# Performance work log

Hardware: AMD Instinct MI355X
Metric: run time of the kernel (lower is better)

Reference implementation:

```python
import jax, jax.numpy as jnp
import numpy as np

N_NODES = 50000
N_EDGES = 800000
D_NODE = 64
D_EDGE = 32
D_OUT = 64


def setup_inputs() -> dict:
    key = jax.random.key(0)
    ks = jax.random.split(key, 8)
    node_feats = jax.random.normal(ks[0], (N_NODES, D_NODE), dtype=jnp.float32)
    edge_feats = jax.random.normal(ks[1], (N_EDGES, D_EDGE), dtype=jnp.float32)
    src = jax.random.randint(ks[2], (N_EDGES,), 0, N_NODES, dtype=jnp.int32)
    dst = jax.random.randint(ks[3], (N_EDGES,), 0, N_NODES, dtype=jnp.int32)
    # f_e: Linear(D_NODE + D_EDGE + D_NODE -> D_OUT), f_v: Linear(D_OUT + D_NODE -> D_OUT)
    d_in_e = D_NODE + D_EDGE + D_NODE
    d_in_v = D_OUT + D_NODE
    W_e = jax.random.normal(ks[4], (d_in_e, D_OUT), dtype=jnp.float32) / np.sqrt(d_in_e)
    b_e = jnp.zeros((D_OUT,), dtype=jnp.float32)
    W_v = jax.random.normal(ks[5], (d_in_v, D_OUT), dtype=jnp.float32) / np.sqrt(d_in_v)
    b_v = jnp.zeros((D_OUT,), dtype=jnp.float32)
    return {"node_feats": node_feats, "edge_feats": edge_feats, "src": src, "dst": dst,
            "W_e": W_e, "b_e": b_e, "W_v": W_v, "b_v": b_v}


def reference(node_feats, edge_feats, src, dst, W_e, b_e, W_v, b_v):
    n_nodes = node_feats.shape[0]
    # Edge update: gather src/dst node feats, concat with edge feats, MLP + ReLU
    x_e = jnp.concatenate([node_feats[src], edge_feats, node_feats[dst]], axis=1)  # [E, 2*Dn+De]
    m = jax.nn.relu(x_e @ W_e + b_e)  # [E, D_OUT]
    # Mean aggregation by destination node (DGL 'mean': 0 for isolated nodes)
    msum = jax.ops.segment_sum(m, dst, num_segments=n_nodes)  # [N, D_OUT]
    deg = jax.ops.segment_sum(jnp.ones((dst.shape[0],), dtype=m.dtype), dst, num_segments=n_nodes)
    neigh = jnp.where(deg[:, None] > 0, msum / jnp.maximum(deg[:, None], 1.0), 0.0)
    # Node update MLP
    x_v = jnp.concatenate([neigh, node_feats], axis=1)  # [N, D_OUT + Dn]
    return jax.nn.relu(x_v @ W_v + b_v)
```

## Files before the change

kernel.cpp:

```cpp
#include <hip/hip_runtime.h>

#define DN 64
#define DE 32
#define DO 64
#define NB 256
#define TP 128
#define CH 8

typedef __attribute__((ext_vector_type(8))) short bf16x8;
typedef __attribute__((ext_vector_type(4))) float f32x4;

__device__ inline unsigned pack_bf16(float a, float b) {
    unsigned ua = __float_as_uint(a), ub = __float_as_uint(b);
    ua = (ua + 0x7fffu + ((ua >> 16) & 1u)) >> 16;
    ub = (ub + 0x7fffu + ((ub >> 16) & 1u)) >> 16;
    return ua | (ub << 16);
}
__device__ inline unsigned short bf16_1(float a) {
    unsigned u = __float_as_uint(a);
    return (unsigned short)((u + 0x7fffu + ((u >> 16) & 1u)) >> 16);
}
__device__ inline float bf16f(unsigned short v) {
    return __uint_as_float((unsigned)v << 16);
}

union bfu { unsigned u[4]; bf16x8 v; };

__global__ void __launch_bounds__(256) pre_hist_kernel(
    const float* __restrict__ node, const float* __restrict__ W_e,
    const int* __restrict__ dst,
    unsigned short* __restrict__ PsB, unsigned short* __restrict__ PdB,
    int* __restrict__ cnt, int* __restrict__ rank_,
    int n_nodes, int n_edges)
{
    const int t    = threadIdx.x;
    const int lane = t & 63;
    const int w    = __builtin_amdgcn_readfirstlane((int)(t >> 6));
    const int l15  = lane & 15;
    const int k0   = (lane >> 4) << 3;

    bfu bS[4][2], bD[4][2];
#pragma unroll
    for (int Nt = 0; Nt < 4; ++Nt) {
        const int col = (Nt << 4) | l15;
#pragma unroll
        for (int ks = 0; ks < 2; ++ks) {
            float ws[8], wd[8];
#pragma unroll
            for (int e = 0; e < 8; ++e) {
                ws[e] = W_e[(ks * 32 + k0 + e) * DO + col];
                wd[e] = W_e[(96 + ks * 32 + k0 + e) * DO + col];
            }
#pragma unroll
            for (int q = 0; q < 4; ++q) {
                bS[Nt][ks].u[q] = pack_bf16(ws[2 * q], ws[2 * q + 1]);
                bD[Nt][ks].u[q] = pack_bf16(wd[2 * q], wd[2 * q + 1]);
            }
        }
    }

    const int row0 = blockIdx.x * 64 + w * 16;
    if (row0 < n_nodes) {
        bfu aF[2];
#pragma unroll
        for (int ks = 0; ks < 2; ++ks) {
            const int r = min(row0 + l15, n_nodes - 1);
            const float* __restrict__ p = node + (size_t)r * DN + ks * 32 + k0;
            const float4 f0 = *(const float4*)p;
            const float4 f1 = *(const float4*)(p + 4);
            aF[ks].u[0] = pack_bf16(f0.x, f0.y);
            aF[ks].u[1] = pack_bf16(f0.z, f0.w);
            aF[ks].u[2] = pack_bf16(f1.x, f1.y);
            aF[ks].u[3] = pack_bf16(f1.z, f1.w);
        }
        const int rb = row0 + ((lane >> 4) << 2);
#pragma unroll
        for (int Nt = 0; Nt < 4; ++Nt) {
            const f32x4 z = {0.f, 0.f, 0.f, 0.f};
            f32x4 aS = __builtin_amdgcn_mfma_f32_16x16x32_bf16(aF[0].v, bS[Nt][0].v, z, 0, 0, 0);
            aS = __builtin_amdgcn_mfma_f32_16x16x32_bf16(aF[1].v, bS[Nt][1].v, aS, 0, 0, 0);
            f32x4 aD = __builtin_amdgcn_mfma_f32_16x16x32_bf16(aF[0].v, bD[Nt][0].v, z, 0, 0, 0);
            aD = __builtin_amdgcn_mfma_f32_16x16x32_bf16(aF[1].v, bD[Nt][1].v, aD, 0, 0, 0);
            const int col = (Nt << 4) | l15;
#pragma unroll
            for (int r = 0; r < 4; ++r) {
                if (rb + r < n_nodes) {
                    PsB[(size_t)(rb + r) * DO + col] = bf16_1(aS[r]);
                    PdB[(size_t)(rb + r) * DO + col] = bf16_1(aD[r]);
                }
            }
        }
    }

    const int gt = blockIdx.x * blockDim.x + t;
    const int nt = gridDim.x * blockDim.x;
    for (int e = gt; e < n_edges; e += nt)
        rank_[e] = atomicAdd(&cnt[dst[e]], 1);
}

__global__ void __launch_bounds__(256) scan_partial(
    const int* __restrict__ cnt, int* __restrict__ local,
    int* __restrict__ bsum, float* __restrict__ msum, int n_nodes)
{
    const int C = (n_nodes + NB - 1) / NB;
    const int t = threadIdx.x, lane = t & 63, w = t >> 6;
    const int i = blockIdx.x * C + t;

    int v = (t < C && i < n_nodes) ? cnt[i] : 0;
    int incl = v;
#pragma unroll
    for (int off = 1; off < 64; off <<= 1) {
        int u = __shfl_up(incl, off, 64);
        if (lane >= off) incl += u;
    }
    __shared__ int ws[4], wo[4];
    if (lane == 63) ws[w] = incl;
    __syncthreads();
    if (t == 0) {
        int r = 0;
#pragma unroll
        for (int q = 0; q < 4; ++q) { wo[q] = r; r += ws[q]; }
        bsum[blockIdx.x] = r;
    }
    __syncthreads();
    if (t < C && i < n_nodes) local[i] = incl - v + wo[w];

    const size_t nf4 = (size_t)n_nodes * DO / 4;
    float4* __restrict__ m4 = (float4*)msum;
    const size_t g0 = (size_t)blockIdx.x * blockDim.x + t;
    const size_t gs = (size_t)gridDim.x * blockDim.x;
    const float4 z4 = make_float4(0.f, 0.f, 0.f, 0.f);
    for (size_t j = g0; j < nf4; j += gs) m4[j] = z4;
}

__global__ void __launch_bounds__(256) scan_final(
    const int* __restrict__ local, const int* __restrict__ bsum,
    int* __restrict__ row_start, int n_nodes)
{
    const int t = threadIdx.x, lane = t & 63, w = t >> 6;
    int v = bsum[t];
    int incl = v;
#pragma unroll
    for (int off = 1; off < 64; off <<= 1) {
        int u = __shfl_up(incl, off, 64);
        if (lane >= off) incl += u;
    }
    __shared__ int ws[4], wo[4];
    if (lane == 63) ws[w] = incl;
    __syncthreads();
    if (t == 0) {
        int r = 0;
#pragma unroll
        for (int q = 0; q < 4; ++q) { wo[q] = r; r += ws[q]; }
    }
    __syncthreads();
    const int excl = incl - v + wo[w];

    __shared__ int blockoff;
    if (t == (int)blockIdx.x) blockoff = excl;
    if (blockIdx.x == NB - 1 && t == NB - 1) row_start[n_nodes] = excl + v;
    __syncthreads();

    const int C = (n_nodes + NB - 1) / NB;
    const int i = blockIdx.x * C + t;
    if (t < C && i < n_nodes)
        row_start[i] = local[i] + blockoff;
}

__global__ void __launch_bounds__(256) scatter_kernel(
    const int* __restrict__ dst, const int* __restrict__ src,
    const int* __restrict__ rank_, const int* __restrict__ row_start,
    int2* __restrict__ csr, int n_edges)
{
    const int e = blockIdx.x * blockDim.x + threadIdx.x;
    if (e < n_edges) {
        const int d = dst[e];
        const int p = row_start[d] + rank_[e];
        csr[p] = make_int2(e, src[e] | (d << 16));
    }
}

__global__ void __launch_bounds__(128) agg_mfma_kernel(
    const float* __restrict__ edge,
    const float* __restrict__ W_e, const float* __restrict__ b_e,
    const unsigned short* __restrict__ PsB, const unsigned short* __restrict__ PdB,
    const int* __restrict__ row_start, const int2* __restrict__ csr,
    float* __restrict__ msum, int n_edges)
{
    __shared__ unsigned lds_m[2][32][68];

    const int t    = threadIdx.x;
    const int lane = t & 63;
    const int wid  = __builtin_amdgcn_readfirstlane((int)(t >> 6));
    const int wbeg = blockIdx.x * TP + wid * 64;
    const int wcnt = min(n_edges - wbeg, 64);
    if (wcnt <= 0) return;

    const int l15 = lane & 15;
    const int k0  = (lane >> 4) << 3;

    bfu bfr[4];
#pragma unroll
    for (int Nt = 0; Nt < 4; ++Nt) {
        const int col = (Nt << 4) | l15;
        float wv[8];
#pragma unroll
        for (int e = 0; e < 8; ++e)
            wv[e] = W_e[(64 + k0 + e) * DO + col];
#pragma unroll
        for (int v2 = 0; v2 < 4; ++v2)
            bfr[Nt].u[v2] = pack_bf16(wv[2 * v2], wv[2 * v2 + 1]);
    }
    const float bj = b_e[lane];

    const int2 my2 = csr[min(wbeg + lane, n_edges - 1)];

#pragma unroll
    for (int Mt = 0; Mt < 4; ++Mt) {
        const int eA = __shfl(my2.x, (Mt << 4) | l15, 64);
        const float* __restrict__ ep = edge + (size_t)(unsigned)eA * DE + k0;
        const float4 f0 = *(const float4*)(ep);
        const float4 f1 = *(const float4*)(ep + 4);
        bfu afr;
        afr.u[0] = pack_bf16(f0.x, f0.y);
        afr.u[1] = pack_bf16(f0.z, f0.w);
        afr.u[2] = pack_bf16(f1.x, f1.y);
        afr.u[3] = pack_bf16(f1.z, f1.w);
        const int rp0 = (Mt << 3) + ((lane >> 4) << 1);
#pragma unroll
        for (int Nt = 0; Nt < 4; ++Nt) {
            f32x4 dz = {0.f, 0.f, 0.f, 0.f};
            f32x4 d = __builtin_amdgcn_mfma_f32_16x16x32_bf16(afr.v, bfr[Nt].v, dz, 0, 0, 0);
            const int col = (Nt << 4) | l15;
            lds_m[wid][rp0][col]     = pack_bf16(d[0], d[1]);
            lds_m[wid][rp0 + 1][col] = pack_bf16(d[2], d[3]);
        }
    }

    float acc = 0.f, bpd = 0.f;
    int cur_d = -1;

#define FLUSH()                                                         \
    {                                                                   \
        if (row_start[cur_d] >= wbeg)                                   \
            msum[(size_t)cur_d * DO + lane] = acc;                      \
        else                                                            \
            unsafeAtomicAdd(&msum[(size_t)cur_d * DO + lane], acc);     \
    }

#define ISSUE(CHK, BUF)                                                 \
    _Pragma("unroll")                                                   \
    for (int q = 0; q < CH; ++q) {                                      \
        const int y = __builtin_amdgcn_readlane(my2.y, (CHK) * CH + q); \
        BUF[q] = PsB[(size_t)(unsigned)(y & 0xffff) * DO + lane];       \
    }

#define CONSUME(CHK, BUF)                                               \
    {                                                                   \
        unsigned um[4];                                                 \
        _Pragma("unroll")                                               \
        for (int h = 0; h < 4; ++h)                                     \
            um[h] = lds_m[wid][(CHK) * 4 + h][lane];                    \
        _Pragma("unroll")                                               \
        for (int q = 0; q < CH; ++q) {                                  \
            const int y = __builtin_amdgcn_readlane(my2.y, (CHK) * CH + q); \
            const int d = (int)(((unsigned)y) >> 16);                   \
            if (d != cur_d) {                                           \
                if (cur_d >= 0) FLUSH();                                \
                acc = 0.f;                                              \
                cur_d = d;                                              \
                bpd = bj + bf16f(PdB[(size_t)(unsigned)d * DO + lane]); \
            }                                                           \
            const unsigned u = um[q >> 1];                              \
            const float mv = (q & 1) ? __uint_as_float(u & 0xffff0000u) \
                                     : __uint_as_float(u << 16);        \
            acc += fmaxf(mv + bpd + __uint_as_float((unsigned)BUF[q] << 16), 0.f); \
        }                                                               \
    }

    if (wcnt == 64) {
        unsigned short pnA[CH], pnB[CH], pnC[CH];
        ISSUE(0, pnA) ISSUE(1, pnB)
        ISSUE(2, pnC) CONSUME(0, pnA)
        ISSUE(3, pnA) CONSUME(1, pnB)
        ISSUE(4, pnB) CONSUME(2, pnC)
        ISSUE(5, pnC) CONSUME(3, pnA)
        ISSUE(6, pnA) CONSUME(4, pnB)
        ISSUE(7, pnB) CONSUME(5, pnC)
        CONSUME(6, pnA)
        CONSUME(7, pnB)
    } else {
        for (int p = 0; p < wcnt; ++p) {
            const int y = __builtin_amdgcn_readlane(my2.y, p);
            const int s = y & 0xffff;
            const int d = (int)(((unsigned)y) >> 16);
            const float ps = bf16f(PsB[(size_t)(unsigned)s * DO + lane]);
            if (d != cur_d) {
                if (cur_d >= 0) FLUSH();
                acc = 0.f;
                cur_d = d;
                bpd = bj + bf16f(PdB[(size_t)(unsigned)d * DO + lane]);
            }
            const unsigned u = lds_m[wid][p >> 1][lane];
            const float mv = (p & 1) ? __uint_as_float(u & 0xffff0000u)
                                     : __uint_as_float(u << 16);
            acc += fmaxf(mv + bpd + ps, 0.f);
        }
    }

    {
        const int sb = row_start[cur_d];
        const int se = row_start[cur_d + 1];
        if (sb >= wbeg && se <= wbeg + wcnt)
            msum[(size_t)cur_d * DO + lane] = acc;
        else
            unsafeAtomicAdd(&msum[(size_t)cur_d * DO + lane], acc);
    }
#undef FLUSH
#undef ISSUE
#undef CONSUME
}

__global__ void __launch_bounds__(256) node_out_kernel(
    const float* __restrict__ node, const float* __restrict__ msum,
    const int* __restrict__ row_start,
    const float* __restrict__ W_v, const float* __restrict__ b_v,
    float* __restrict__ out, int n_nodes)
{
    const int t    = threadIdx.x;
    const int lane = t & 63;
    const int w    = __builtin_amdgcn_readfirstlane((int)(t >> 6));
    const int l15  = lane & 15;
    const int k0   = (lane >> 4) << 3;

    bfu bT[4][2], bB[4][2];
#pragma unroll
    for (int Nt = 0; Nt < 4; ++Nt) {
        const int col = (Nt << 4) | l15;
#pragma unroll
        for (int ks = 0; ks < 2; ++ks) {
            float wt[8], wb[8];
#pragma unroll
            for (int e = 0; e < 8; ++e) {
                wt[e] = W_v[(ks * 32 + k0 + e) * DO + col];
                wb[e] = W_v[(64 + ks * 32 + k0 + e) * DO + col];
            }
#pragma unroll
            for (int q = 0; q < 4; ++q) {
                bT[Nt][ks].u[q] = pack_bf16(wt[2 * q], wt[2 * q + 1]);
                bB[Nt][ks].u[q] = pack_bf16(wb[2 * q], wb[2 * q + 1]);
            }
        }
    }

    const int row0 = blockIdx.x * 64 + w * 16;
    if (row0 >= n_nodes) return;

    bfu aM[2], aN[2];
#pragma unroll
    for (int ks = 0; ks < 2; ++ks) {
        const int r = min(row0 + l15, n_nodes - 1);
        const float* __restrict__ pm = msum + (size_t)r * DO + ks * 32 + k0;
        const float* __restrict__ pn = node + (size_t)r * DN + ks * 32 + k0;
        const float4 m0 = *(const float4*)pm;
        const float4 m1 = *(const float4*)(pm + 4);
        const float4 n0 = *(const float4*)pn;
        const float4 n1 = *(const float4*)(pn + 4);
        aM[ks].u[0] = pack_bf16(m0.x, m0.y);
        aM[ks].u[1] = pack_bf16(m0.z, m0.w);
        aM[ks].u[2] = pack_bf16(m1.x, m1.y);
        aM[ks].u[3] = pack_bf16(m1.z, m1.w);
        aN[ks].u[0] = pack_bf16(n0.x, n0.y);
        aN[ks].u[1] = pack_bf16(n0.z, n0.w);
        aN[ks].u[2] = pack_bf16(n1.x, n1.y);
        aN[ks].u[3] = pack_bf16(n1.z, n1.w);
    }

    f32x4 accT[4], accB[4];
#pragma unroll
    for (int Nt = 0; Nt < 4; ++Nt) {
        const f32x4 z = {0.f, 0.f, 0.f, 0.f};
        f32x4 aT = __builtin_amdgcn_mfma_f32_16x16x32_bf16(aM[0].v, bT[Nt][0].v, z, 0, 0, 0);
        aT = __builtin_amdgcn_mfma_f32_16x16x32_bf16(aM[1].v, bT[Nt][1].v, aT, 0, 0, 0);
        f32x4 aB = __builtin_amdgcn_mfma_f32_16x16x32_bf16(aN[0].v, bB[Nt][0].v, z, 0, 0, 0);
        aB = __builtin_amdgcn_mfma_f32_16x16x32_bf16(aN[1].v, bB[Nt][1].v, aB, 0, 0, 0);
        accT[Nt] = aT;
        accB[Nt] = aB;
    }

    const int rb = row0 + ((lane >> 4) << 2);
#pragma unroll
    for (int r = 0; r < 4; ++r) {
        const int row = rb + r;
        if (row < n_nodes) {
            const float dg = (float)(row_start[row + 1] - row_start[row]);
            const float inv = (dg > 0.f) ? 1.f / dg : 0.f;
#pragma unroll
            for (int Nt = 0; Nt < 4; ++Nt) {
                const int col = (Nt << 4) | l15;
                const float val = accT[Nt][r] * inv + accB[Nt][r] + b_v[col];
                out[(size_t)row * DO + col] = fmaxf(val, 0.f);
            }
        }
    }
}

extern "C" void kernel_launch(void* const* d_in, const int* in_sizes, int n_in,
                              void* d_out, int out_size, void* d_ws, size_t ws_size,
                              hipStream_t stream)
{
    const float* node = (const float*)d_in[0];
    const float* edge = (const float*)d_in[1];
    const int*   src  = (const int*)d_in[2];
    const int*   dst  = (const int*)d_in[3];
    const float* W_e  = (const float*)d_in[4];
    const float* b_e  = (const float*)d_in[5];
    const float* W_v  = (const float*)d_in[6];
    const float* b_v  = (const float*)d_in[7];
    float* out = (float*)d_out;

    const int n_nodes = in_sizes[0] / DN;
    const int n_edges = in_sizes[2];
    const int ntiles  = (n_nodes + 63) / 64;

    unsigned short* PsB = (unsigned short*)d_ws;
    unsigned short* PdB = PsB + (size_t)n_nodes * DO;
    float* msum = (float*)(PdB + (size_t)n_nodes * DO);
    int* cnt       = (int*)(msum + (size_t)n_nodes * DO);
    int* row_start = cnt + n_nodes;
    int* local     = row_start + (n_nodes + 1);
    int* bsum      = local + n_nodes;
    int* rank_     = bsum + NB;
    int2* csr      = (int2*)(((size_t)(rank_ + n_edges) + 15) & ~(size_t)15);

    hipMemsetAsync(cnt, 0, (size_t)n_nodes * sizeof(int), stream);

    pre_hist_kernel<<<ntiles, 256, 0, stream>>>(node, W_e, dst, PsB, PdB,
                                                cnt, rank_, n_nodes, n_edges);
    scan_partial<<<NB, 256, 0, stream>>>(cnt, local, bsum, msum, n_nodes);
    scan_final<<<NB, 256, 0, stream>>>(local, bsum, row_start, n_nodes);
    scatter_kernel<<<(n_edges + 255) / 256, 256, 0, stream>>>(dst, src, rank_, row_start,
                                                              csr, n_edges);
    agg_mfma_kernel<<<(n_edges + TP - 1) / TP, 128, 0, stream>>>(edge, W_e, b_e, PsB, PdB,
                                                                 row_start, csr, msum, n_edges);
    node_out_kernel<<<ntiles, 256, 0, stream>>>(node, msum, row_start, W_v, b_v,
                                                out, n_nodes);
}
```

Baseline: 134.2 us.

## Fuse scan-final into scatter and split edge MFMA into two interleaved halves

```diff
diff --git a/kernel.cpp b/kernel.cpp
--- a/kernel.cpp
+++ b/kernel.cpp
@@ -133,49 +133,47 @@
     for (size_t j = g0; j < nf4; j += gs) m4[j] = z4;
 }
 
-__global__ void __launch_bounds__(256) scan_final(
-    const int* __restrict__ local, const int* __restrict__ bsum,
-    int* __restrict__ row_start, int n_nodes)
-{
+__global__ void __launch_bounds__(256) scatter_scan_kernel(
+    const int* __restrict__ dst, const int* __restrict__ src,
+    const int* __restrict__ rank_, const int* __restrict__ local,
+    const int* __restrict__ bsum,
+    int* __restrict__ row_start, int2* __restrict__ csr,
+    int n_nodes, int n_edges, int C)
+{
+    __shared__ int boff[NB];
     const int t = threadIdx.x, lane = t & 63, w = t >> 6;
-    int v = bsum[t];
-    int incl = v;
-#pragma unroll
-    for (int off = 1; off < 64; off <<= 1) {
-        int u = __shfl_up(incl, off, 64);
-        if (lane >= off) incl += u;
-    }
-    __shared__ int ws[4], wo[4];
-    if (lane == 63) ws[w] = incl;
+
+    {
+        int v = bsum[t];
+        int incl = v;
+#pragma unroll
+        for (int off = 1; off < 64; off <<= 1) {
+            int u = __shfl_up(incl, off, 64);
+            if (lane >= off) incl += u;
+        }
+        __shared__ int ws[4], wo[4];
+        if (lane == 63) ws[w] = incl;
+        __syncthreads();
+        if (t == 0) {
+            int r = 0;
+#pragma unroll
+            for (int q = 0; q < 4; ++q) { wo[q] = r; r += ws[q]; }
+        }
+        __syncthreads();
+        boff[t] = incl - v + wo[w];
+    }
     __syncthreads();
-    if (t == 0) {
-        int r = 0;
-#pragma unroll
-        for (int q = 0; q < 4; ++q) { wo[q] = r; r += ws[q]; }
-    }
-    __syncthreads();
-    const int excl = incl - v + wo[w];
-
-    __shared__ int blockoff;
-    if (t == (int)blockIdx.x) blockoff = excl;
-    if (blockIdx.x == NB - 1 && t == NB - 1) row_start[n_nodes] = excl + v;
-    __syncthreads();
-
-    const int C = (n_nodes + NB - 1) / NB;
-    const int i = blockIdx.x * C + t;
-    if (t < C && i < n_nodes)
-        row_start[i] = local[i] + blockoff;
-}
-
-__global__ void __launch_bounds__(256) scatter_kernel(
-    const int* __restrict__ dst, const int* __restrict__ src,
-    const int* __restrict__ rank_, const int* __restrict__ row_start,
-    int2* __restrict__ csr, int n_edges)
-{
-    const int e = blockIdx.x * blockDim.x + threadIdx.x;
+
+    if (blockIdx.x < NB) {
+        const int i = blockIdx.x * C + t;
+        if (t < C && i < n_nodes) row_start[i] = local[i] + boff[blockIdx.x];
+        if (blockIdx.x == 0 && t == 0) row_start[n_nodes] = n_edges;
+    }
+
+    const int e = blockIdx.x * blockDim.x + t;
     if (e < n_edges) {
         const int d = dst[e];
-        const int p = row_start[d] + rank_[e];
+        const int p = local[d] + boff[(unsigned)d / (unsigned)C] + rank_[e];
         csr[p] = make_int2(e, src[e] | (d << 16));
     }
 }
@@ -187,7 +185,7 @@
     const int* __restrict__ row_start, const int2* __restrict__ csr,
     float* __restrict__ msum, int n_edges)
 {
-    __shared__ unsigned lds_m[2][32][68];
+    __shared__ unsigned lds_m[2][16][68];
 
     const int t    = threadIdx.x;
     const int lane = t & 63;
@@ -215,30 +213,31 @@
 
     const int2 my2 = csr[min(wbeg + lane, n_edges - 1)];
 
-#pragma unroll
-    for (int Mt = 0; Mt < 4; ++Mt) {
-        const int eA = __shfl(my2.x, (Mt << 4) | l15, 64);
-        const float* __restrict__ ep = edge + (size_t)(unsigned)eA * DE + k0;
-        const float4 f0 = *(const float4*)(ep);
-        const float4 f1 = *(const float4*)(ep + 4);
-        bfu afr;
-        afr.u[0] = pack_bf16(f0.x, f0.y);
-        afr.u[1] = pack_bf16(f0.z, f0.w);
-        afr.u[2] = pack_bf16(f1.x, f1.y);
-        afr.u[3] = pack_bf16(f1.z, f1.w);
-        const int rp0 = (Mt << 3) + ((lane >> 4) << 1);
-#pragma unroll
-        for (int Nt = 0; Nt < 4; ++Nt) {
-            f32x4 dz = {0.f, 0.f, 0.f, 0.f};
-            f32x4 d = __builtin_amdgcn_mfma_f32_16x16x32_bf16(afr.v, bfr[Nt].v, dz, 0, 0, 0);
-            const int col = (Nt << 4) | l15;
-            lds_m[wid][rp0][col]     = pack_bf16(d[0], d[1]);
-            lds_m[wid][rp0 + 1][col] = pack_bf16(d[2], d[3]);
-        }
-    }
-
     float acc = 0.f, bpd = 0.f;
     int cur_d = -1;
+
+#define MFMA_HALF(H)                                                          \
+    _Pragma("unroll")                                                         \
+    for (int Mt = 2 * (H); Mt < 2 * (H) + 2; ++Mt) {                          \
+        const int eA = __shfl(my2.x, (Mt << 4) | l15, 64);                    \
+        const float* __restrict__ ep = edge + (size_t)(unsigned)eA * DE + k0; \
+        const float4 f0 = *(const float4*)(ep);                               \
+        const float4 f1 = *(const float4*)(ep + 4);                           \
+        bfu afr;                                                              \
+        afr.u[0] = pack_bf16(f0.x, f0.y);                                     \
+        afr.u[1] = pack_bf16(f0.z, f0.w);                                     \
+        afr.u[2] = pack_bf16(f1.x, f1.y);                                     \
+        afr.u[3] = pack_bf16(f1.z, f1.w);                                     \
+        const int rp0 = ((Mt & 1) << 3) + ((lane >> 4) << 1);                 \
+        _Pragma("unroll")                                                     \
+        for (int Nt = 0; Nt < 4; ++Nt) {                                      \
+            f32x4 dz = {0.f, 0.f, 0.f, 0.f};                                  \
+            f32x4 d = __builtin_amdgcn_mfma_f32_16x16x32_bf16(afr.v, bfr[Nt].v, dz, 0, 0, 0); \
+            const int col = (Nt << 4) | l15;                                  \
+            lds_m[wid][rp0][col]     = pack_bf16(d[0], d[1]);                 \
+            lds_m[wid][rp0 + 1][col] = pack_bf16(d[2], d[3]);                 \
+        }                                                                     \
+    }
 
 #define FLUSH()                                                         \
     {                                                                   \
@@ -260,7 +259,7 @@
         unsigned um[4];                                                 \
         _Pragma("unroll")                                               \
         for (int h = 0; h < 4; ++h)                                     \
-            um[h] = lds_m[wid][(CHK) * 4 + h][lane];                    \
+            um[h] = lds_m[wid][((CHK) & 3) * 4 + h][lane];              \
         _Pragma("unroll")                                               \
         for (int q = 0; q < CH; ++q) {                                  \
             const int y = __builtin_amdgcn_readlane(my2.y, (CHK) * CH + q); \
@@ -280,31 +279,39 @@
 
     if (wcnt == 64) {
         unsigned short pnA[CH], pnB[CH], pnC[CH];
-        ISSUE(0, pnA) ISSUE(1, pnB)
-        ISSUE(2, pnC) CONSUME(0, pnA)
+        MFMA_HALF(0)
+        ISSUE(0, pnA) ISSUE(1, pnB) ISSUE(2, pnC)
+        CONSUME(0, pnA)
         ISSUE(3, pnA) CONSUME(1, pnB)
         ISSUE(4, pnB) CONSUME(2, pnC)
         ISSUE(5, pnC) CONSUME(3, pnA)
+        MFMA_HALF(1)
         ISSUE(6, pnA) CONSUME(4, pnB)
         ISSUE(7, pnB) CONSUME(5, pnC)
         CONSUME(6, pnA)
         CONSUME(7, pnB)
     } else {
-        for (int p = 0; p < wcnt; ++p) {
-            const int y = __builtin_amdgcn_readlane(my2.y, p);
-            const int s = y & 0xffff;
-            const int d = (int)(((unsigned)y) >> 16);
-            const float ps = bf16f(PsB[(size_t)(unsigned)s * DO + lane]);
-            if (d != cur_d) {
-                if (cur_d >= 0) FLUSH();
-                acc = 0.f;
-                cur_d = d;
-                bpd = bj + bf16f(PdB[(size_t)(unsigned)d * DO + lane]);
-            }
-            const unsigned u = lds_m[wid][p >> 1][lane];
-            const float mv = (p & 1) ? __uint_as_float(u & 0xffff0000u)
-                                     : __uint_as_float(u << 16);
-            acc += fmaxf(mv + bpd + ps, 0.f);
+        for (int h = 0; h < 2; ++h) {
+            const int p0 = h * 32;
+            if (p0 >= wcnt) break;
+            MFMA_HALF(h)
+            const int pe = min(wcnt, p0 + 32);
+            for (int p = p0; p < pe; ++p) {
+                const int y = __builtin_amdgcn_readlane(my2.y, p);
+                const int s = y & 0xffff;
+                const int d = (int)(((unsigned)y) >> 16);
+                const float ps = bf16f(PsB[(size_t)(unsigned)s * DO + lane]);
+                if (d != cur_d) {
+                    if (cur_d >= 0) FLUSH();
+                    acc = 0.f;
+                    cur_d = d;
+                    bpd = bj + bf16f(PdB[(size_t)(unsigned)d * DO + lane]);
+                }
+                const unsigned u = lds_m[wid][(p & 31) >> 1][lane];
+                const float mv = (p & 1) ? __uint_as_float(u & 0xffff0000u)
+                                         : __uint_as_float(u << 16);
+                acc += fmaxf(mv + bpd + ps, 0.f);
+            }
         }
     }
 
@@ -316,6 +323,7 @@
         else
             unsafeAtomicAdd(&msum[(size_t)cur_d * DO + lane], acc);
     }
+#undef MFMA_HALF
 #undef FLUSH
 #undef ISSUE
 #undef CONSUME
@@ -422,6 +430,7 @@
     const int n_nodes = in_sizes[0] / DN;
     const int n_edges = in_sizes[2];
     const int ntiles  = (n_nodes + 63) / 64;
+    const int C       = (n_nodes + NB - 1) / NB;
 
     unsigned short* PsB = (unsigned short*)d_ws;
     unsigned short* PdB = PsB + (size_t)n_nodes * DO;
@@ -438,9 +447,8 @@
     pre_hist_kernel<<<ntiles, 256, 0, stream>>>(node, W_e, dst, PsB, PdB,
                                                 cnt, rank_, n_nodes, n_edges);
     scan_partial<<<NB, 256, 0, stream>>>(cnt, local, bsum, msum, n_nodes);
-    scan_final<<<NB, 256, 0, stream>>>(local, bsum, row_start, n_nodes);
-    scatter_kernel<<<(n_edges + 255) / 256, 256, 0, stream>>>(dst, src, rank_, row_start,
-                                                              csr, n_edges);
+    scatter_scan_kernel<<<(n_edges + 255) / 256, 256, 0, stream>>>(
+        dst, src, rank_, local, bsum, row_start, csr, n_nodes, n_edges, C);
     agg_mfma_kernel<<<(n_edges + TP - 1) / TP, 128, 0, stream>>>(edge, W_e, b_e, PsB, PdB,
                                                                  row_start, csr, msum, n_edges);
     node_out_kernel<<<ntiles, 256, 0, stream>>>(node, msum, row_start, W_v, b_v,
```

New measurement: 133.4 us. No clear change (-0.6%).
